# Kernel tuning notes

Measured on AMD Instinct MI355X. Metric: run time of the kernel, lower is better.

## Reference

```python
import jax, jax.numpy as jnp
import numpy as np

VAR_EPS = 1e-05


def setup_inputs() -> dict:
    key = jax.random.key(0)
    k1, k2 = jax.random.split(key)
    B, T = 1024, 16384
    pred = jax.random.normal(k1, (B, T), dtype=jnp.float32)
    target = jax.random.normal(k2, (B, T), dtype=jnp.float32)
    return {"pred": pred, "target": target}


def reference(pred, target):
    # Per-row Pearson correlation, vectorized over the batch dimension.
    T = pred.shape[1]
    mp = jnp.mean(pred, axis=1, keepdims=True)
    mt = jnp.mean(target, axis=1, keepdims=True)
    cp = pred - mp                      # [B, T] centered
    ct = target - mt
    sp = jnp.sum(cp * cp, axis=1)       # [B] sum of squares
    st = jnp.sum(ct * ct, axis=1)
    num = jnp.sum(cp * ct, axis=1)      # [B] covariance numerator
    # torch.var uses unbiased estimator (correction=1)
    var_p = sp / (T - 1)
    var_t = st / (T - 1)
    denom = jnp.sqrt(sp * st)
    safe_denom = jnp.where(denom > 0, denom, 1.0)
    corr = num / safe_denom
    valid = (var_p > VAR_EPS) & (var_t > VAR_EPS) & (denom > 0) & ~jnp.isnan(corr)
    per_row = jnp.where(valid, 1.0 - corr, 1.0)
    return jnp.mean(per_row)
```

## Files before the change

kernel.cpp:

```cpp
#include <hip/hip_runtime.h>

#define T_LEN 16384
#define VAR_EPS 1e-5f

typedef float v4 __attribute__((ext_vector_type(4)));
#define NTL(P) __builtin_nontemporal_load(P)


#define ACC(P,Q)                                              \
    sp  += (P.x + P.y) + (P.z + P.w);                         \
    st  += (Q.x + Q.y) + (Q.z + Q.w);                         \
    spp += P.x*P.x + P.y*P.y + P.z*P.z + P.w*P.w;             \
    stt += Q.x*Q.x + Q.y*Q.y + Q.z*Q.z + Q.w*Q.w;             \
    spt += P.x*Q.x + P.y*Q.y + P.z*Q.z + P.w*Q.w;

__global__ __launch_bounds__(256) void pearson_row_kernel(
    const float* __restrict__ pred, const float* __restrict__ target,
    float* __restrict__ moments)
{
    const int row = blockIdx.x;
    const int tid = threadIdx.x;

    const v4* __restrict__ p4 = (const v4*)(pred   + (size_t)row * T_LEN);
    const v4* __restrict__ t4 = (const v4*)(target + (size_t)row * T_LEN);

    float sp = 0.f, st = 0.f, spp = 0.f, stt = 0.f, spt = 0.f;

    v4 P[4], Q[4];

    #pragma unroll
    for (int s = 0; s < 4; ++s) {
        P[s] = NTL(p4 + tid + 256 * s);
        Q[s] = NTL(t4 + tid + 256 * s);
    }

    #pragma unroll
    for (int i = 0; i < 12; ++i) {
        ACC(P[i & 3], Q[i & 3]);
        P[i & 3] = NTL(p4 + tid + 256 * (i + 4));
        Q[i & 3] = NTL(t4 + tid + 256 * (i + 4));
    }

    #pragma unroll
    for (int i = 12; i < 16; ++i) {
        ACC(P[i & 3], Q[i & 3]);
    }

    #pragma unroll
    for (int off = 32; off > 0; off >>= 1) {
        sp  += __shfl_down(sp,  off);
        st  += __shfl_down(st,  off);
        spp += __shfl_down(spp, off);
        stt += __shfl_down(stt, off);
        spt += __shfl_down(spt, off);
    }

    __shared__ float ws[4][8];
    const int wid = tid >> 6;
    if ((tid & 63) == 0) {
        ws[wid][0] = sp;  ws[wid][1] = st;  ws[wid][2] = spp;
        ws[wid][3] = stt; ws[wid][4] = spt;
    }
    __syncthreads();

    if (tid == 0) {
        float* m = moments + (size_t)row * 8;
        m[0] = ws[0][0] + ws[1][0] + ws[2][0] + ws[3][0];
        m[1] = ws[0][1] + ws[1][1] + ws[2][1] + ws[3][1];
        m[2] = ws[0][2] + ws[1][2] + ws[2][2] + ws[3][2];
        m[3] = ws[0][3] + ws[1][3] + ws[2][3] + ws[3][3];
        m[4] = ws[0][4] + ws[1][4] + ws[2][4] + ws[3][4];
    }
}

__global__ __launch_bounds__(1024) void pearson_final_kernel(
    const float* __restrict__ moments, float* __restrict__ out, int B)
{
    const int tid = threadIdx.x;
    float loss_sum = 0.f;

    for (int r = tid; r < B; r += 1024) {
        const float* m = moments + (size_t)r * 8;
        float S_p  = m[0];
        float S_t  = m[1];
        float S_pp = m[2];
        float S_tt = m[3];
        float S_pt = m[4];

        const float T   = (float)T_LEN;
        const float inv = 1.0f / T;
        float cp2 = S_pp - S_p * S_p * inv;
        float ct2 = S_tt - S_t * S_t * inv;
        float num = S_pt - S_p * S_t * inv;

        float var_p = cp2 / (T - 1.0f);
        float var_t = ct2 / (T - 1.0f);
        float denom = sqrtf(cp2 * ct2);
        float safe  = (denom > 0.0f) ? denom : 1.0f;
        float corr  = num / safe;
        bool valid = (var_p > VAR_EPS) && (var_t > VAR_EPS) &&
                     (denom > 0.0f) && !isnan(corr);
        loss_sum += valid ? (1.0f - corr) : 1.0f;
    }

    #pragma unroll
    for (int off = 32; off > 0; off >>= 1)
        loss_sum += __shfl_down(loss_sum, off);

    __shared__ float ws[16];
    if ((tid & 63) == 0) ws[tid >> 6] = loss_sum;
    __syncthreads();

    if (tid == 0) {
        float tot = 0.f;
        #pragma unroll
        for (int w = 0; w < 16; ++w) tot += ws[w];
        out[0] = tot / (float)B;
    }
}

extern "C" void kernel_launch(void* const* d_in, const int* in_sizes, int n_in,
                              void* d_out, int out_size, void* d_ws, size_t ws_size,
                              hipStream_t stream) {
    const float* pred   = (const float*)d_in[0];
    const float* target = (const float*)d_in[1];
    float* out     = (float*)d_out;
    float* moments = (float*)d_ws;

    const int B = in_sizes[0] / T_LEN;

    pearson_row_kernel<<<B, 256, 0, stream>>>(pred, target, moments);
    pearson_final_kernel<<<1, 1024, 0, stream>>>(moments, out, B);
}
```

Baseline: 137.2 us.

## Stream row data through LDS with async global_load_lds in a 4-stage pipeline

Replaces the register-prefetched nontemporal vector loads with direct global-to-LDS loads (global_load_lds, 16 bytes per lane), staged through a per-wave 4-slot ring buffer with three chunks in flight. Explicit vmcnt waits and inline ds_read_b128 pull each chunk back into registers for the moment accumulation. Each wave now processes one contiguous quarter of the row rather than interleaved strides. The intent is more bytes in flight and lower VGPR pressure, at the cost of 64 KB of LDS per block, which limits occupancy, plus an extra LDS round trip and fragile hand-counted waitcnts.

After: 143.2 us. 1.04x slower.

```diff
diff --git a/kernel.cpp b/kernel.cpp
--- a/kernel.cpp
+++ b/kernel.cpp
@@ -4,7 +4,10 @@
 #define VAR_EPS 1e-5f
 
 typedef float v4 __attribute__((ext_vector_type(4)));
-#define NTL(P) __builtin_nontemporal_load(P)
+
+typedef __attribute__((address_space(1))) const void GV;
+typedef __attribute__((address_space(3))) void       LV;
+typedef __attribute__((address_space(3))) float      LF;
 
 
 #define ACC(P,Q)                                              \
@@ -18,33 +21,59 @@
     const float* __restrict__ pred, const float* __restrict__ target,
     float* __restrict__ moments)
 {
-    const int row = blockIdx.x;
-    const int tid = threadIdx.x;
+    __shared__ float lds[4][4][1024];
 
-    const v4* __restrict__ p4 = (const v4*)(pred   + (size_t)row * T_LEN);
-    const v4* __restrict__ t4 = (const v4*)(target + (size_t)row * T_LEN);
+    const int row  = blockIdx.x;
+    const int tid  = threadIdx.x;
+    const int wid  = tid >> 6;
+    const int lane = tid & 63;
+
+    const float* pw = pred   + (size_t)row * T_LEN + wid * 4096;
+    const float* tw = target + (size_t)row * T_LEN + wid * 4096;
+
+#define STAGE(c) do {                                                         \
+    const int s_ = (c) & 3;                                                   \
+    __builtin_amdgcn_global_load_lds((GV*)(pw + (c)*512       + lane*4),      \
+                                     (LV*)&lds[wid][s_][0],   16, 0, 0);      \
+    __builtin_amdgcn_global_load_lds((GV*)(pw + (c)*512 + 256 + lane*4),      \
+                                     (LV*)&lds[wid][s_][256], 16, 0, 0);      \
+    __builtin_amdgcn_global_load_lds((GV*)(tw + (c)*512       + lane*4),      \
+                                     (LV*)&lds[wid][s_][512], 16, 0, 0);      \
+    __builtin_amdgcn_global_load_lds((GV*)(tw + (c)*512 + 256 + lane*4),      \
+                                     (LV*)&lds[wid][s_][768], 16, 0, 0);      \
+  } while (0)
+
+    const unsigned lane_base =
+        (unsigned)(size_t)((LF*)&lds[wid][0][0]) + (unsigned)lane * 32u;
 
     float sp = 0.f, st = 0.f, spp = 0.f, stt = 0.f, spt = 0.f;
 
-    v4 P[4], Q[4];
+    STAGE(0); STAGE(1); STAGE(2);
 
     #pragma unroll
-    for (int s = 0; s < 4; ++s) {
-        P[s] = NTL(p4 + tid + 256 * s);
-        Q[s] = NTL(t4 + tid + 256 * s);
+    for (int c = 0; c < 8; ++c) {
+        if      (c <= 5) asm volatile("s_waitcnt vmcnt(8)" ::: "memory");
+        else if (c == 6) asm volatile("s_waitcnt vmcnt(4)" ::: "memory");
+        else             asm volatile("s_waitcnt vmcnt(0)" ::: "memory");
+        __builtin_amdgcn_sched_barrier(0);
+
+        const unsigned a = lane_base + (unsigned)((c & 3) * 4096);
+        v4 P0, P1, Q0, Q1;
+        asm volatile(
+            "ds_read_b128 %0, %4\n\t"
+            "ds_read_b128 %1, %4 offset:16\n\t"
+            "ds_read_b128 %2, %4 offset:2048\n\t"
+            "ds_read_b128 %3, %4 offset:2064\n\t"
+            "s_waitcnt lgkmcnt(0)"
+            : "=&v"(P0), "=&v"(P1), "=&v"(Q0), "=&v"(Q1)
+            : "v"(a) : "memory");
+
+        ACC(P0, Q0);
+        ACC(P1, Q1);
+
+        if (c < 5) STAGE(c + 3);
     }
-
-    #pragma unroll
-    for (int i = 0; i < 12; ++i) {
-        ACC(P[i & 3], Q[i & 3]);
-        P[i & 3] = NTL(p4 + tid + 256 * (i + 4));
-        Q[i & 3] = NTL(t4 + tid + 256 * (i + 4));
-    }
-
-    #pragma unroll
-    for (int i = 12; i < 16; ++i) {
-        ACC(P[i & 3], Q[i & 3]);
-    }
+#undef STAGE
 
     #pragma unroll
     for (int off = 32; off > 0; off >>= 1) {
@@ -55,21 +84,22 @@
         spt += __shfl_down(spt, off);
     }
 
-    __shared__ float ws[4][8];
-    const int wid = tid >> 6;
+    __syncthreads();
+    float* wsf = (float*)&lds[0][0][0];
     if ((tid & 63) == 0) {
-        ws[wid][0] = sp;  ws[wid][1] = st;  ws[wid][2] = spp;
-        ws[wid][3] = stt; ws[wid][4] = spt;
+        wsf[wid * 8 + 0] = sp;  wsf[wid * 8 + 1] = st;
+        wsf[wid * 8 + 2] = spp; wsf[wid * 8 + 3] = stt;
+        wsf[wid * 8 + 4] = spt;
     }
     __syncthreads();
 
     if (tid == 0) {
         float* m = moments + (size_t)row * 8;
-        m[0] = ws[0][0] + ws[1][0] + ws[2][0] + ws[3][0];
-        m[1] = ws[0][1] + ws[1][1] + ws[2][1] + ws[3][1];
-        m[2] = ws[0][2] + ws[1][2] + ws[2][2] + ws[3][2];
-        m[3] = ws[0][3] + ws[1][3] + ws[2][3] + ws[3][3];
-        m[4] = ws[0][4] + ws[1][4] + ws[2][4] + ws[3][4];
+        m[0] = wsf[0] + wsf[8]  + wsf[16] + wsf[24];
+        m[1] = wsf[1] + wsf[9]  + wsf[17] + wsf[25];
+        m[2] = wsf[2] + wsf[10] + wsf[18] + wsf[26];
+        m[3] = wsf[3] + wsf[11] + wsf[19] + wsf[27];
+        m[4] = wsf[4] + wsf[12] + wsf[20] + wsf[28];
     }
 }
 
```
